# Kernel tuning notes

Hardware: AMD Instinct MI355X
Metric: run time of the kernel (lower is better)

The kernel has to match this reference:

```python
import jax, jax.numpy as jnp
import numpy as np

N, E = 100000, 1600000
F_IN, HID, C, L = 512, 128, 64, 64
ALPHA, THETA = 0.1, 0.5


def setup_inputs() -> dict:
    key = jax.random.key(0)
    ks = jax.random.split(key, 6)
    x = jax.random.normal(ks[0], (N, F_IN), jnp.float32)
    edge_index = jax.random.randint(ks[1], (2, E), 0, N, jnp.int32)
    W_in = jax.random.normal(ks[2], (F_IN, HID), jnp.float32) * (1.0 / np.sqrt(F_IN))
    b_in = jnp.zeros((HID,), jnp.float32)
    W_convs = jax.random.normal(ks[3], (L, HID, HID), jnp.float32) * (1.0 / np.sqrt(HID))
    W_out = jax.random.normal(ks[4], (HID, C), jnp.float32) * (1.0 / np.sqrt(HID))
    b_out = jnp.zeros((C,), jnp.float32)
    return {"x": x, "edge_index": edge_index, "W_in": W_in, "b_in": b_in,
            "W_convs": W_convs, "W_out": W_out, "b_out": b_out}


def reference(x, edge_index, W_in, b_in, W_convs, W_out, b_out):
    src, dst = edge_index[0], edge_index[1]
    # gcn_norm with self loops: A_hat = D^-1/2 (A + I) D^-1/2
    deg = jax.ops.segment_sum(jnp.ones((E,), x.dtype), dst, num_segments=N) + 1.0
    dinv = jax.lax.rsqrt(deg)
    ew = dinv[src] * dinv[dst]          # [E] off-diagonal weights
    self_w = dinv * dinv                # [N] self-loop weights

    def spmm(h):  # h: [N, HID]
        agg = jax.ops.segment_sum(h[src] * ew[:, None], dst, num_segments=N)
        return agg + self_w[:, None] * h

    # beta_l = log(theta / l + 1), l = 1..L
    betas = jnp.log(THETA / jnp.arange(1, L + 1, dtype=x.dtype) + 1.0)

    x0 = jax.nn.relu(x @ W_in + b_in)   # [N, HID]

    def layer(h, lw):
        W, beta = lw
        p = spmm(h)
        t = (1.0 - ALPHA) * p + ALPHA * x0          # initial residual
        out = (1.0 - beta) * t + beta * (t @ W)     # identity mapping (shared weights)
        return jax.nn.relu(out), None

    z, _ = jax.lax.scan(layer, x0, (W_convs, betas))
    logits = z @ W_out + b_out
    return z, jax.nn.log_softmax(logits, axis=-1)
```

## Files before the change

kernel.cpp:

```cpp
#include <hip/hip_runtime.h>
#include <hip/hip_bf16.h>

#define NN 100000
#define NE 1600000
#define F_IN 512
#define HID 128
#define C_OUT 64
#define L_LAYERS 64
#define SCAN_NB 98

using short8 = __attribute__((ext_vector_type(8))) short;
using f32x4  = __attribute__((ext_vector_type(4))) float;
typedef __attribute__((ext_vector_type(4))) unsigned short ushort4v;

__device__ __forceinline__ short f2bf(float f) {
    __hip_bfloat16 h = __float2bfloat16(f);
    return __builtin_bit_cast(short, h);
}
__device__ __forceinline__ unsigned short f2bfu(float f) {
    __hip_bfloat16 h = __float2bfloat16(f);
    return __builtin_bit_cast(unsigned short, h);
}
__device__ __forceinline__ float bflo(unsigned u) { return __uint_as_float(u << 16); }
__device__ __forceinline__ float bfhi(unsigned u) { return __uint_as_float(u & 0xffff0000u); }
__device__ __forceinline__ float bf2f(unsigned short u) { return __uint_as_float((unsigned)u << 16); }


__global__ void count_deg(const int* __restrict__ dst, int* __restrict__ cnt) {
    int e = blockIdx.x * blockDim.x + threadIdx.x;
    if (e < NE) atomicAdd(&cnt[dst[e]], 1);
}

__global__ void compute_dinv(const int* __restrict__ cnt, float* __restrict__ dinv) {
    int n = blockIdx.x * blockDim.x + threadIdx.x;
    if (n < NN) dinv[n] = rsqrtf((float)cnt[n] + 1.0f);
}

__global__ __launch_bounds__(256) void scan1(const int* __restrict__ cnt,
                                             int* __restrict__ row_ptr,
                                             int* __restrict__ partial) {
    __shared__ int sdata[256];
    int tid = threadIdx.x;
    int base = blockIdx.x * 1024;
    int v[4];
    int idx0 = base + tid * 4;
#pragma unroll
    for (int i = 0; i < 4; ++i) {
        int idx = idx0 + i;
        v[i] = (idx < NN) ? cnt[idx] : 0;
    }
    int s = v[0] + v[1] + v[2] + v[3];
    sdata[tid] = s;
    __syncthreads();
    int x = s;
    for (int off = 1; off < 256; off <<= 1) {
        int y = (tid >= off) ? sdata[tid - off] : 0;
        __syncthreads();
        x += y;
        sdata[tid] = x;
        __syncthreads();
    }
    int run = x - s;
#pragma unroll
    for (int i = 0; i < 4; ++i) {
        int idx = idx0 + i;
        if (idx < NN) row_ptr[idx] = run;
        run += v[i];
    }
    if (tid == 255) partial[blockIdx.x] = x;
}

__global__ __launch_bounds__(128) void scan2(int* __restrict__ partial) {
    __shared__ int sdata[128];
    int tid = threadIdx.x;
    int v = (tid < SCAN_NB) ? partial[tid] : 0;
    sdata[tid] = v;
    __syncthreads();
    int x = v;
    for (int off = 1; off < 128; off <<= 1) {
        int y = (tid >= off) ? sdata[tid - off] : 0;
        __syncthreads();
        x += y;
        sdata[tid] = x;
        __syncthreads();
    }
    if (tid < SCAN_NB) partial[tid] = x - v;
}

__global__ void scan3(int* __restrict__ row_ptr, const int* __restrict__ partial) {
    int idx = blockIdx.x * blockDim.x + threadIdx.x;
    if (idx < NN) row_ptr[idx] += partial[idx >> 10];
    else if (idx <= NN + 64) row_ptr[idx] = NE;
}

__global__ void scatter_csr(const int* __restrict__ src, const int* __restrict__ dst,
                            const float* __restrict__ dinv, int* __restrict__ fill,
                            int2* __restrict__ edges) {
    int e = blockIdx.x * blockDim.x + threadIdx.x;
    if (e >= NE) return;
    int s = src[e], d = dst[e];
    int pos = atomicAdd(&fill[d], 1);
    edges[pos] = make_int2(s, __float_as_int(dinv[s] * dinv[d]));
}

__global__ __launch_bounds__(256) void prep_wt(const float* __restrict__ Wc,
                                               const float* __restrict__ Win,
                                               __hip_bfloat16* __restrict__ WT,
                                               __hip_bfloat16* __restrict__ WinT) {
    int b = blockIdx.x, tid = threadIdx.x;
    if (b < 64) {
        const float* src = Wc + (size_t)b * HID * HID;
        __hip_bfloat16* dstp = WT + (size_t)b * HID * HID;
        for (int it = 0; it < 64; ++it) {
            int idx = it * 256 + tid;
            int n = idx >> 7, k = idx & 127;
            dstp[idx] = __float2bfloat16(src[k * HID + n]);
        }
    } else {
        int j = b - 64;
        for (int it = 0; it < 16; ++it) {
            int gid = j * 4096 + it * 256 + tid;
            int n = gid >> 9, k = gid & 511;
            WinT[gid] = __float2bfloat16(Win[k * HID + n]);
        }
    }
}

__global__ __launch_bounds__(256) void gemm_x0_mfma(const float* __restrict__ X,
                                                    const __hip_bfloat16* __restrict__ WinT,
                                                    const float* __restrict__ bias,
                                                    __hip_bfloat16* __restrict__ X0b) {
    __shared__ short SMEM[128 * 128];
    int tid = threadIdx.x;
    int w = tid >> 6, l = tid & 63, g = l >> 4, r = l & 15;
    int row0 = blockIdx.x * 128;
    f32x4 acc[2][8] = {};

    float4 sx0[2], sx1[2];
    uint4 sw[2];
    auto load_regs = [&](int kt) {
        int k0 = kt * 32;
#pragma unroll
        for (int i = 0; i < 2; ++i) {
            int id = i * 256 + tid;
            int rr = id >> 2, slot = id & 3;
            int grow = row0 + rr;
            sx0[i] = make_float4(0.f, 0.f, 0.f, 0.f); sx1[i] = sx0[i];
            if (grow < NN) {
                sx0[i] = *(const float4*)&X[(size_t)grow * F_IN + k0 + slot * 8];
                sx1[i] = *(const float4*)&X[(size_t)grow * F_IN + k0 + slot * 8 + 4];
            }
            sw[i] = *(const uint4*)&WinT[(size_t)rr * F_IN + k0 + slot * 8];
        }
    };

    load_regs(0);
    for (int kt = 0; kt < 16; ++kt) {
        short* Xs = SMEM + (kt & 1) * 4096;
        short* Wsh = SMEM + 8192 + (kt & 1) * 4096;
#pragma unroll
        for (int i = 0; i < 2; ++i) {
            int id = i * 256 + tid;
            int rr = id >> 2, slot = id & 3;
            short8 p;
            p[0] = f2bf(sx0[i].x); p[1] = f2bf(sx0[i].y); p[2] = f2bf(sx0[i].z); p[3] = f2bf(sx0[i].w);
            p[4] = f2bf(sx1[i].x); p[5] = f2bf(sx1[i].y); p[6] = f2bf(sx1[i].z); p[7] = f2bf(sx1[i].w);
            *(short8*)&Xs[rr * 32 + (slot ^ ((rr >> 1) & 3)) * 8] = p;
            *(uint4*)&Wsh[rr * 32 + (slot ^ ((rr >> 1) & 3)) * 8] = sw[i];
        }
        __syncthreads();
        if (kt < 15) load_regs(kt + 1);
        short8 a[2], bb[8];
#pragma unroll
        for (int m = 0; m < 2; ++m) {
            int row = w * 32 + m * 16 + r;
            a[m] = *(short8*)&Xs[row * 32 + (g ^ ((row >> 1) & 3)) * 8];
        }
#pragma unroll
        for (int n = 0; n < 8; ++n) {
            int row = n * 16 + r;
            bb[n] = *(short8*)&Wsh[row * 32 + (g ^ ((row >> 1) & 3)) * 8];
        }
#pragma unroll
        for (int m = 0; m < 2; ++m)
#pragma unroll
            for (int n = 0; n < 8; ++n)
                acc[m][n] = __builtin_amdgcn_mfma_f32_16x16x32_bf16(a[m], bb[n], acc[m][n], 0, 0, 0);
    }
    __syncthreads();
#pragma unroll
    for (int m = 0; m < 2; ++m) {
#pragma unroll
        for (int n = 0; n < 8; ++n) {
            int col = n * 16 + r;
            float bv = bias[col];
#pragma unroll
            for (int q = 0; q < 4; ++q) {
                int row = w * 32 + m * 16 + g * 4 + q;
                float v = fmaxf(acc[m][n][q] + bv, 0.f);
                SMEM[row * 128 + ((col >> 3) ^ (row & 15)) * 8 + (col & 7)] = f2bf(v);
            }
        }
    }
    __syncthreads();
#pragma unroll
    for (int i = 0; i < 8; ++i) {
        int id = i * 256 + tid;
        int rr = id >> 4, c8 = id & 15;
        int grow = row0 + rr;
        if (grow < NN)
            *(uint4*)&X0b[(size_t)grow * HID + c8 * 8] =
                *(uint4*)&SMEM[rr * 128 + ((c8 ^ (rr & 15)) * 8)];
    }
}

__global__ __launch_bounds__(512, 6) void layer_fused(const unsigned* __restrict__ H2,
                                                      const unsigned* __restrict__ X02,
                                                      const float* __restrict__ dinv,
                                                      const int* __restrict__ row_ptr,
                                                      const int2* __restrict__ edges,
                                                      const __hip_bfloat16* __restrict__ WTl,
                                                      float beta,
                                                      __hip_bfloat16* __restrict__ Hout,
                                                      float* __restrict__ Zf) {
    __shared__ short Ts[64 * 128];
    __shared__ short Ws[128 * 128];
    int tid = threadIdx.x;
    int w = tid >> 6, l = tid & 63, g = l >> 4, r = l & 15;
    int row0 = blockIdx.x * 64;

#pragma unroll
    for (int i = 0; i < 4; ++i) {
        int id = i * 512 + tid;
        int rr = id >> 4, slot = id & 15;
        uint4 wv = *(const uint4*)&WTl[(size_t)id * 8];
        *(uint4*)&Ws[rr * 128 + (slot ^ (rr & 15)) * 8] = wv;
    }

    unsigned* TsU = (unsigned*)Ts;
    int nb0 = row0 + w * 8;
    int ep[9];
#pragma unroll
    for (int k = 0; k < 9; ++k) ep[k] = __builtin_amdgcn_readfirstlane(row_ptr[nb0 + k]);

#pragma unroll
    for (int j = 0; j < 4; ++j) {
        int rrA = w * 8 + 2 * j, rrB = rrA + 1;
        int nA = row0 + rrA, nB = nA + 1;
        bool vA = nA < NN, vB = nB < NN;
        unsigned hsA = vA ? H2[((unsigned)nA << 6) + l] : 0u;
        unsigned hsB = vB ? H2[((unsigned)nB << 6) + l] : 0u;
        unsigned xvA = vA ? X02[((unsigned)nA << 6) + l] : 0u;
        unsigned xvB = vB ? X02[((unsigned)nB << 6) + l] : 0u;
        float dvA = vA ? dinv[nA] : 0.f, dvB = vB ? dinv[nB] : 0.f;
        float a0A = dvA * dvA * bflo(hsA), a1A = dvA * dvA * bfhi(hsA);
        float a0B = dvB * dvB * bflo(hsB), a1B = dvB * dvB * bfhi(hsB);
        int eA = ep[2 * j], e1A = ep[2 * j + 1];
        int eB = e1A, e1B = ep[2 * j + 2];
        while (eA < e1A || eB < e1B) {
            int cA = e1A - eA; cA = cA > 8 ? 8 : (cA < 0 ? 0 : cA);
            int cB = e1B - eB; cB = cB > 8 ? 8 : (cB < 0 ? 0 : cB);
            int sA[8], sB[8];
            float wA[8], wB[8];
#pragma unroll
            for (int u = 0; u < 8; ++u) {
                int2 t = edges[eA + u];
                sA[u] = (u < cA) ? t.x : 0;
                wA[u] = (u < cA) ? __int_as_float(t.y) : 0.f;
            }
#pragma unroll
            for (int u = 0; u < 8; ++u) {
                int2 t = edges[eB + u];
                sB[u] = (u < cB) ? t.x : 0;
                wB[u] = (u < cB) ? __int_as_float(t.y) : 0.f;
            }
            unsigned hvA[8], hvB[8];
#pragma unroll
            for (int u = 0; u < 8; ++u) hvA[u] = H2[((unsigned)sA[u] << 6) + l];
#pragma unroll
            for (int u = 0; u < 8; ++u) hvB[u] = H2[((unsigned)sB[u] << 6) + l];
#pragma unroll
            for (int u = 0; u < 8; ++u) {
                a0A = fmaf(wA[u], bflo(hvA[u]), a0A);
                a1A = fmaf(wA[u], bfhi(hvA[u]), a1A);
                a0B = fmaf(wB[u], bflo(hvB[u]), a0B);
                a1B = fmaf(wB[u], bfhi(hvB[u]), a1B);
            }
            eA += cA; eB += cB;
        }
        a0A = 0.9f * a0A + 0.1f * bflo(xvA);  a1A = 0.9f * a1A + 0.1f * bfhi(xvA);
        a0B = 0.9f * a0B + 0.1f * bflo(xvB);  a1B = 0.9f * a1B + 0.1f * bfhi(xvB);
        unsigned pkA = (unsigned)f2bfu(a0A) | ((unsigned)f2bfu(a1A) << 16);
        unsigned pkB = (unsigned)f2bfu(a0B) | ((unsigned)f2bfu(a1B) << 16);
        TsU[rrA * 64 + ((l >> 2) ^ (rrA & 15)) * 4 + (l & 3)] = pkA;
        TsU[rrB * 64 + ((l >> 2) ^ (rrB & 15)) * 4 + (l & 3)] = pkB;
    }
    __syncthreads();

    int nb = w & 3, cg = w >> 2;
    f32x4 acc[4] = {};
#pragma unroll
    for (int ks = 0; ks < 4; ++ks) {
        int rrT = nb * 16 + r;
        short8 bT = *(short8*)&Ts[rrT * 128 + ((ks * 4 + g) ^ (rrT & 15)) * 8];
        short8 aW[4];
#pragma unroll
        for (int c = 0; c < 4; ++c) {
            int rrW = (cg * 4 + c) * 16 + r;
            aW[c] = *(short8*)&Ws[rrW * 128 + ((ks * 4 + g) ^ (rrW & 15)) * 8];
        }
#pragma unroll
        for (int c = 0; c < 4; ++c)
            acc[c] = __builtin_amdgcn_mfma_f32_16x16x32_bf16(aW[c], bT, acc[c], 0, 0, 0);
    }

    float omb = 1.0f - beta;
    int node = nb * 16 + r;
    int grow = row0 + node;
    if (grow < NN) {
#pragma unroll
        for (int c = 0; c < 4; ++c) {
            int c0 = (cg * 4 + c) * 16 + g * 4;
            int slotE = c0 >> 3, posE = c0 & 7;
            ushort4v tv = *(ushort4v*)&Ts[node * 128 + (slotE ^ (node & 15)) * 8 + posE];
            float o[4];
#pragma unroll
            for (int q = 0; q < 4; ++q)
                o[q] = fmaxf(omb * bf2f(tv[q]) + beta * acc[c][q], 0.f);
            if (Zf) {
                *(float4*)&Zf[(size_t)grow * HID + c0] = make_float4(o[0], o[1], o[2], o[3]);
            } else {
                ushort4v hv;
#pragma unroll
                for (int q = 0; q < 4; ++q) hv[q] = f2bfu(o[q]);
                *(ushort4v*)&Hout[(size_t)grow * HID + c0] = hv;
            }
        }
    }
}

__global__ __launch_bounds__(64) void final_kernel(const float* __restrict__ Z,
                                                   const float* __restrict__ Wout,
                                                   const float* __restrict__ bout,
                                                   float* __restrict__ lo) {
    int n = blockIdx.x;
    int c = threadIdx.x;
    float logit = bout[c];
    for (int k = 0; k < HID; ++k) {
        logit = fmaf(Z[(size_t)n * HID + k], Wout[k * C_OUT + c], logit);
    }
    float m = logit;
#pragma unroll
    for (int off = 32; off; off >>= 1) m = fmaxf(m, __shfl_xor(m, off));
    float ex = __expf(logit - m);
    float ssum = ex;
#pragma unroll
    for (int off = 32; off; off >>= 1) ssum += __shfl_xor(ssum, off);
    lo[(size_t)n * C_OUT + c] = logit - m - logf(ssum);
}

extern "C" void kernel_launch(void* const* d_in, const int* in_sizes, int n_in,
                              void* d_out, int out_size, void* d_ws, size_t ws_size,
                              hipStream_t stream) {
    const float* x = (const float*)d_in[0];
    const int* ei = (const int*)d_in[1];
    const int* src = ei;
    const int* dst = ei + NE;
    const float* W_in = (const float*)d_in[2];
    const float* b_in = (const float*)d_in[3];
    const float* W_convs = (const float*)d_in[4];
    const float* W_out = (const float*)d_in[5];
    const float* b_out = (const float*)d_in[6];
    float* out = (float*)d_out;

    char* ws = (char*)d_ws;
    float* dinv = (float*)ws;              ws += (size_t)NN * 4;
    int* row_ptr = (int*)ws;               ws += (size_t)(NN + 72) * 4;
    int* fill = (int*)ws;                  ws += (size_t)NN * 4;
    int* partial = (int*)ws;               ws += (size_t)128 * 4;
    int2* edges = (int2*)ws;               ws += (size_t)(NE + 8) * 8;
    __hip_bfloat16* WT = (__hip_bfloat16*)ws;   ws += (size_t)L_LAYERS * HID * HID * 2;
    __hip_bfloat16* WinT = (__hip_bfloat16*)ws; ws += (size_t)F_IN * HID * 2;
    __hip_bfloat16* x0b = (__hip_bfloat16*)ws;  ws += (size_t)NN * HID * 2;
    __hip_bfloat16* HbA = (__hip_bfloat16*)ws;  ws += (size_t)NN * HID * 2;
    __hip_bfloat16* HbB = (__hip_bfloat16*)ws;  ws += (size_t)NN * HID * 2;

    hipMemsetAsync(fill, 0, (size_t)NN * 4, stream);
    count_deg<<<(NE + 255) / 256, 256, 0, stream>>>(dst, fill);
    compute_dinv<<<(NN + 255) / 256, 256, 0, stream>>>(fill, dinv);
    scan1<<<SCAN_NB, 256, 0, stream>>>(fill, row_ptr, partial);
    scan2<<<1, 128, 0, stream>>>(partial);
    scan3<<<(NN + 255) / 256, 256, 0, stream>>>(row_ptr, partial);
    hipMemcpyAsync(fill, row_ptr, (size_t)NN * 4, hipMemcpyDeviceToDevice, stream);
    scatter_csr<<<(NE + 255) / 256, 256, 0, stream>>>(src, dst, dinv, fill, edges);
    prep_wt<<<80, 256, 0, stream>>>(W_convs, W_in, WT, WinT);

    int gemm_blocks = (NN + 127) / 128;
    gemm_x0_mfma<<<gemm_blocks, 256, 0, stream>>>(x, WinT, b_in, x0b);

    int layer_blocks = (NN + 63) / 64;
    float* zf = out;
    for (int l = 0; l < L_LAYERS; ++l) {
        const __hip_bfloat16* h_in = (l == 0) ? x0b : ((l & 1) ? HbA : HbB);
        __hip_bfloat16* h_out = (l & 1) ? HbB : HbA;
        float beta = logf(0.5f / (float)(l + 1) + 1.0f);
        bool last = (l == L_LAYERS - 1);
        layer_fused<<<layer_blocks, 512, 0, stream>>>(
            (const unsigned*)h_in, (const unsigned*)x0b, dinv, row_ptr, edges,
            WT + (size_t)l * HID * HID, beta,
            h_out, last ? zf : (float*)nullptr);
    }

    final_kernel<<<NN, 64, 0, stream>>>(zf, W_out, b_out, out + (size_t)NN * HID);
}
```

Baseline: 6.369 ms.

## Deepen x0 GEMM prefetch, widen SpMM gather unroll, tile final logits kernel

The input GEMM now keeps two register sets of prefetched tiles and loads two k-steps ahead, which raises memory-level parallelism. The per-layer SpMM gather loop processes up to 12 edges per batch instead of 8, with the edge buffer padding enlarged to match. The final log-softmax kernel is rewritten to stage W_out and 64 rows of Z in shared memory and compute four nodes per wave, replacing one 64-thread block per node. Together these aim to hide load latency and cut launch and global-read overhead, at the cost of higher register use and more wasted lanes on low-degree nodes.

```diff
diff --git a/kernel.cpp b/kernel.cpp
--- a/kernel.cpp
+++ b/kernel.cpp
@@ -126,6 +126,59 @@
     }
 }
 
+#define LOAD_SET(X0V, X1V, WVV, KT)                                              \
+    {                                                                            \
+        int k0_ = (KT) * 32;                                                     \
+        _Pragma("unroll")                                                        \
+        for (int i = 0; i < 2; ++i) {                                            \
+            int id = i * 256 + tid;                                              \
+            int rr = id >> 2, slot = id & 3;                                     \
+            int grow = row0 + rr;                                                \
+            X0V[i] = make_float4(0.f, 0.f, 0.f, 0.f); X1V[i] = X0V[i];           \
+            if (grow < NN) {                                                     \
+                X0V[i] = *(const float4*)&X[(size_t)grow * F_IN + k0_ + slot * 8];     \
+                X1V[i] = *(const float4*)&X[(size_t)grow * F_IN + k0_ + slot * 8 + 4]; \
+            }                                                                    \
+            WVV[i] = *(const uint4*)&WinT[(size_t)rr * F_IN + k0_ + slot * 8];   \
+        }                                                                        \
+    }
+
+#define PHASE(X0V, X1V, WVV, KT, BUF)                                            \
+    {                                                                            \
+        short* Xs = SMEM + (BUF) * 4096;                                         \
+        short* Wsh = SMEM + 8192 + (BUF) * 4096;                                 \
+        _Pragma("unroll")                                                        \
+        for (int i = 0; i < 2; ++i) {                                            \
+            int id = i * 256 + tid;                                              \
+            int rr = id >> 2, slot = id & 3;                                     \
+            short8 p;                                                            \
+            p[0] = f2bf(X0V[i].x); p[1] = f2bf(X0V[i].y);                        \
+            p[2] = f2bf(X0V[i].z); p[3] = f2bf(X0V[i].w);                        \
+            p[4] = f2bf(X1V[i].x); p[5] = f2bf(X1V[i].y);                        \
+            p[6] = f2bf(X1V[i].z); p[7] = f2bf(X1V[i].w);                        \
+            *(short8*)&Xs[rr * 32 + (slot ^ ((rr >> 1) & 3)) * 8] = p;           \
+            *(uint4*)&Wsh[rr * 32 + (slot ^ ((rr >> 1) & 3)) * 8] = WVV[i];      \
+        }                                                                        \
+        __syncthreads();                                                         \
+        if ((KT) < 14) LOAD_SET(X0V, X1V, WVV, (KT) + 2);                        \
+        short8 a[2], bb[8];                                                      \
+        _Pragma("unroll")                                                        \
+        for (int m = 0; m < 2; ++m) {                                            \
+            int row = w * 32 + m * 16 + r;                                       \
+            a[m] = *(short8*)&Xs[row * 32 + (g ^ ((row >> 1) & 3)) * 8];         \
+        }                                                                        \
+        _Pragma("unroll")                                                        \
+        for (int n = 0; n < 8; ++n) {                                            \
+            int row = n * 16 + r;                                                \
+            bb[n] = *(short8*)&Wsh[row * 32 + (g ^ ((row >> 1) & 3)) * 8];       \
+        }                                                                        \
+        _Pragma("unroll")                                                        \
+        for (int m = 0; m < 2; ++m)                                              \
+            _Pragma("unroll")                                                    \
+            for (int n = 0; n < 8; ++n)                                          \
+                acc[m][n] = __builtin_amdgcn_mfma_f32_16x16x32_bf16(a[m], bb[n], acc[m][n], 0, 0, 0); \
+    }
+
 __global__ __launch_bounds__(256) void gemm_x0_mfma(const float* __restrict__ X,
                                                     const __hip_bfloat16* __restrict__ WinT,
                                                     const float* __restrict__ bias,
@@ -136,56 +189,14 @@
     int row0 = blockIdx.x * 128;
     f32x4 acc[2][8] = {};
 
-    float4 sx0[2], sx1[2];
-    uint4 sw[2];
-    auto load_regs = [&](int kt) {
-        int k0 = kt * 32;
-#pragma unroll
-        for (int i = 0; i < 2; ++i) {
-            int id = i * 256 + tid;
-            int rr = id >> 2, slot = id & 3;
-            int grow = row0 + rr;
-            sx0[i] = make_float4(0.f, 0.f, 0.f, 0.f); sx1[i] = sx0[i];
-            if (grow < NN) {
-                sx0[i] = *(const float4*)&X[(size_t)grow * F_IN + k0 + slot * 8];
-                sx1[i] = *(const float4*)&X[(size_t)grow * F_IN + k0 + slot * 8 + 4];
-            }
-            sw[i] = *(const uint4*)&WinT[(size_t)rr * F_IN + k0 + slot * 8];
-        }
-    };
-
-    load_regs(0);
-    for (int kt = 0; kt < 16; ++kt) {
-        short* Xs = SMEM + (kt & 1) * 4096;
-        short* Wsh = SMEM + 8192 + (kt & 1) * 4096;
-#pragma unroll
-        for (int i = 0; i < 2; ++i) {
-            int id = i * 256 + tid;
-            int rr = id >> 2, slot = id & 3;
-            short8 p;
-            p[0] = f2bf(sx0[i].x); p[1] = f2bf(sx0[i].y); p[2] = f2bf(sx0[i].z); p[3] = f2bf(sx0[i].w);
-            p[4] = f2bf(sx1[i].x); p[5] = f2bf(sx1[i].y); p[6] = f2bf(sx1[i].z); p[7] = f2bf(sx1[i].w);
-            *(short8*)&Xs[rr * 32 + (slot ^ ((rr >> 1) & 3)) * 8] = p;
-            *(uint4*)&Wsh[rr * 32 + (slot ^ ((rr >> 1) & 3)) * 8] = sw[i];
-        }
-        __syncthreads();
-        if (kt < 15) load_regs(kt + 1);
-        short8 a[2], bb[8];
-#pragma unroll
-        for (int m = 0; m < 2; ++m) {
-            int row = w * 32 + m * 16 + r;
-            a[m] = *(short8*)&Xs[row * 32 + (g ^ ((row >> 1) & 3)) * 8];
-        }
-#pragma unroll
-        for (int n = 0; n < 8; ++n) {
-            int row = n * 16 + r;
-            bb[n] = *(short8*)&Wsh[row * 32 + (g ^ ((row >> 1) & 3)) * 8];
-        }
-#pragma unroll
-        for (int m = 0; m < 2; ++m)
-#pragma unroll
-            for (int n = 0; n < 8; ++n)
-                acc[m][n] = __builtin_amdgcn_mfma_f32_16x16x32_bf16(a[m], bb[n], acc[m][n], 0, 0, 0);
+    float4 ax0[2], ax1[2]; uint4 aw[2];
+    float4 bx0[2], bx1[2]; uint4 bw[2];
+
+    LOAD_SET(ax0, ax1, aw, 0);
+    LOAD_SET(bx0, bx1, bw, 1);
+    for (int kt = 0; kt < 16; kt += 2) {
+        PHASE(ax0, ax1, aw, kt, 0);
+        PHASE(bx0, bx1, bw, kt + 1, 1);
     }
     __syncthreads();
 #pragma unroll
@@ -258,29 +269,29 @@
         int eA = ep[2 * j], e1A = ep[2 * j + 1];
         int eB = e1A, e1B = ep[2 * j + 2];
         while (eA < e1A || eB < e1B) {
-            int cA = e1A - eA; cA = cA > 8 ? 8 : (cA < 0 ? 0 : cA);
-            int cB = e1B - eB; cB = cB > 8 ? 8 : (cB < 0 ? 0 : cB);
-            int sA[8], sB[8];
-            float wA[8], wB[8];
-#pragma unroll
-            for (int u = 0; u < 8; ++u) {
+            int cA = e1A - eA; cA = cA > 12 ? 12 : (cA < 0 ? 0 : cA);
+            int cB = e1B - eB; cB = cB > 12 ? 12 : (cB < 0 ? 0 : cB);
+            int sA[12], sB[12];
+            float wA[12], wB[12];
+#pragma unroll
+            for (int u = 0; u < 12; ++u) {
                 int2 t = edges[eA + u];
                 sA[u] = (u < cA) ? t.x : 0;
                 wA[u] = (u < cA) ? __int_as_float(t.y) : 0.f;
             }
 #pragma unroll
-            for (int u = 0; u < 8; ++u) {
+            for (int u = 0; u < 12; ++u) {
                 int2 t = edges[eB + u];
                 sB[u] = (u < cB) ? t.x : 0;
                 wB[u] = (u < cB) ? __int_as_float(t.y) : 0.f;
             }
-            unsigned hvA[8], hvB[8];
-#pragma unroll
-            for (int u = 0; u < 8; ++u) hvA[u] = H2[((unsigned)sA[u] << 6) + l];
-#pragma unroll
-            for (int u = 0; u < 8; ++u) hvB[u] = H2[((unsigned)sB[u] << 6) + l];
-#pragma unroll
-            for (int u = 0; u < 8; ++u) {
+            unsigned hvA[12], hvB[12];
+#pragma unroll
+            for (int u = 0; u < 12; ++u) hvA[u] = H2[((unsigned)sA[u] << 6) + l];
+#pragma unroll
+            for (int u = 0; u < 12; ++u) hvB[u] = H2[((unsigned)sB[u] << 6) + l];
+#pragma unroll
+            for (int u = 0; u < 12; ++u) {
                 a0A = fmaf(wA[u], bflo(hvA[u]), a0A);
                 a1A = fmaf(wA[u], bfhi(hvA[u]), a1A);
                 a0B = fmaf(wB[u], bflo(hvB[u]), a0B);
@@ -339,24 +350,58 @@
     }
 }
 
-__global__ __launch_bounds__(64) void final_kernel(const float* __restrict__ Z,
-                                                   const float* __restrict__ Wout,
-                                                   const float* __restrict__ bout,
-                                                   float* __restrict__ lo) {
-    int n = blockIdx.x;
-    int c = threadIdx.x;
-    float logit = bout[c];
-    for (int k = 0; k < HID; ++k) {
-        logit = fmaf(Z[(size_t)n * HID + k], Wout[k * C_OUT + c], logit);
-    }
-    float m = logit;
-#pragma unroll
-    for (int off = 32; off; off >>= 1) m = fmaxf(m, __shfl_xor(m, off));
-    float ex = __expf(logit - m);
-    float ssum = ex;
-#pragma unroll
-    for (int off = 32; off; off >>= 1) ssum += __shfl_xor(ssum, off);
-    lo[(size_t)n * C_OUT + c] = logit - m - logf(ssum);
+__global__ __launch_bounds__(256) void final_kernel(const float* __restrict__ Z,
+                                                    const float* __restrict__ Wout,
+                                                    const float* __restrict__ bout,
+                                                    float* __restrict__ lo) {
+    __shared__ float Wl[128 * 64];
+    __shared__ float Zl[64][128];
+    int tid = threadIdx.x;
+    int w = tid >> 6, c = tid & 63;
+    int n0 = blockIdx.x * 64;
+#pragma unroll
+    for (int i = 0; i < 8; ++i) {
+        int id = i * 256 + tid;
+        *(float4*)&Wl[id * 4] = *(const float4*)&Wout[(size_t)id * 4];
+    }
+#pragma unroll
+    for (int i = 0; i < 8; ++i) {
+        int id = i * 256 + tid;
+        int rr = id >> 5, c4 = id & 31;
+        int n = n0 + rr;
+        float4 v = make_float4(0.f, 0.f, 0.f, 0.f);
+        if (n < NN) v = *(const float4*)&Z[(size_t)n * HID + c4 * 4];
+        *(float4*)&Zl[rr][c4 * 4] = v;
+    }
+    __syncthreads();
+    float bv = bout[c];
+#pragma unroll
+    for (int i = 0; i < 4; ++i) {
+        int nodeb = i * 16 + w * 4;
+        float l0 = 0.f, l1 = 0.f, l2 = 0.f, l3 = 0.f;
+#pragma unroll 8
+        for (int k = 0; k < 128; ++k) {
+            float wv = Wl[k * 64 + c];
+            l0 = fmaf(Zl[nodeb + 0][k], wv, l0);
+            l1 = fmaf(Zl[nodeb + 1][k], wv, l1);
+            l2 = fmaf(Zl[nodeb + 2][k], wv, l2);
+            l3 = fmaf(Zl[nodeb + 3][k], wv, l3);
+        }
+        float lg[4] = {l0 + bv, l1 + bv, l2 + bv, l3 + bv};
+#pragma unroll
+        for (int j = 0; j < 4; ++j) {
+            float logit = lg[j];
+            float m = logit;
+#pragma unroll
+            for (int off = 32; off; off >>= 1) m = fmaxf(m, __shfl_xor(m, off));
+            float ex = __expf(logit - m);
+            float ssum = ex;
+#pragma unroll
+            for (int off = 32; off; off >>= 1) ssum += __shfl_xor(ssum, off);
+            int n = n0 + nodeb + j;
+            if (n < NN) lo[(size_t)n * C_OUT + c] = logit - m - logf(ssum);
+        }
+    }
 }
 
 extern "C" void kernel_launch(void* const* d_in, const int* in_sizes, int n_in,
@@ -378,7 +423,7 @@
     int* row_ptr = (int*)ws;               ws += (size_t)(NN + 72) * 4;
     int* fill = (int*)ws;                  ws += (size_t)NN * 4;
     int* partial = (int*)ws;               ws += (size_t)128 * 4;
-    int2* edges = (int2*)ws;               ws += (size_t)(NE + 8) * 8;
+    int2* edges = (int2*)ws;               ws += (size_t)(NE + 32) * 8;
     __hip_bfloat16* WT = (__hip_bfloat16*)ws;   ws += (size_t)L_LAYERS * HID * HID * 2;
     __hip_bfloat16* WinT = (__hip_bfloat16*)ws; ws += (size_t)F_IN * HID * 2;
     __hip_bfloat16* x0b = (__hip_bfloat16*)ws;  ws += (size_t)NN * HID * 2;
@@ -411,5 +456,5 @@
             h_out, last ? zf : (float*)nullptr);
     }
 
-    final_kernel<<<NN, 64, 0, stream>>>(zf, W_out, b_out, out + (size_t)NN * HID);
-}
+    final_kernel<<<(NN + 63) / 64, 256, 0, stream>>>(zf, W_out, b_out, out + (size_t)NN * HID);
+}
```

After: 6.349 ms. About the same (-0.3%).
